# Optimization experiments

Hardware: AMD Instinct MI355X
Metric: run time of the kernel (lower is better)

Reference implementation:

```python
import jax, jax.numpy as jnp
import numpy as np
from jax import lax

RANK = 2
INPUT_SIZE = 8
HIDDEN_SIZE = 1024
NUM_MIXTURES = 4
ALPHA = 0.1
BASE_SCALE = 500.0
D = 2 * RANK + INPUT_SIZE  # 12
BATCH, SEQ_LEN = 64, 512


def setup_inputs() -> dict:
    key = jax.random.key(0)
    k1, k2, k3, k4, k5 = jax.random.split(key, 5)
    return {
        "x": jax.random.normal(k1, (BATCH, SEQ_LEN, INPUT_SIZE), jnp.float32),
        "eps": jax.random.normal(k2, (NUM_MIXTURES, HIDDEN_SIZE, D), jnp.float32),
        "means": jax.random.normal(k3, (NUM_MIXTURES, D), jnp.float32),
        "scale_tril_raw": jax.random.normal(k4, (NUM_MIXTURES, D, D), jnp.float32) / np.sqrt(HIDDEN_SIZE),
        "mixture_weights": jax.random.uniform(k5, (NUM_MIXTURES,), jnp.float32),
    }


def reference(x, eps, means, scale_tril_raw, mixture_weights):
    # _clamp_tril: lower-triangular with strictly positive diagonal
    diag = jnp.abs(jnp.diagonal(scale_tril_raw, axis1=-2, axis2=-1) - 1e-12) + 1e-12  # [K,D]
    L = jnp.tril(scale_tril_raw, -1) + diag[..., None] * jnp.eye(D, dtype=scale_tril_raw.dtype)
    # _normalize_weights
    w = jnp.clip(mixture_weights, 1e-6, None)
    w = w / jnp.sum(w)
    # rsample: mean + eps @ L^T, per mixture -> [K, H, D]
    samp = means[:, None, :] + jnp.einsum('khd,ked->khe', eps, L)
    mixed = jnp.einsum('k,khd->hd', w, samp)  # weighted sum over mixtures [H, D]
    m = mixed[:, :RANK]            # [H, r]
    n = mixed[:, RANK:2 * RANK]    # [H, r]
    I = mixed[:, 2 * RANK:]        # [H, input_size]
    J = (m @ n.T) * (BASE_SCALE / HIDDEN_SIZE)  # [H, H]
    span = jnp.concatenate([m, I], axis=1)      # [H, r + input_size]

    def step(h, x_t):
        dh = -h + jnp.tanh(h) @ J.T + x_t @ I.T
        h_new = h + ALPHA * dh
        return h_new, h_new

    h0 = jnp.zeros((x.shape[0], HIDDEN_SIZE), x.dtype)
    _, hs = lax.scan(step, h0, jnp.swapaxes(x, 0, 1))  # hs: [T, B, H]
    hiddens = jnp.swapaxes(hs, 0, 1)                   # [B, T, H]
    pinv = jnp.linalg.pinv(span)                       # [r+input_size, H]
    return jnp.einsum('dh,bth->btd', pinv, hiddens)    # [B, T, r+input_size]
```

## Files before the change

### kernel.cpp

```cpp
#include <hip/hip_runtime.h>

#define HS   1024
#define SEQ  512
#define NBAT 64
#define INSZ 8
#define NM   4
#define DD   12

#define DPP_ADD(v, ctrl, rmask, bmask) \
  v += __int_as_float(__builtin_amdgcn_update_dpp(0, __float_as_int(v), ctrl, rmask, bmask, true))

__device__ __forceinline__ void wave64_sum2(float &a, float &b){
  DPP_ADD(a, 0x111, 0xf, 0xf); DPP_ADD(b, 0x111, 0xf, 0xf);
  DPP_ADD(a, 0x112, 0xf, 0xf); DPP_ADD(b, 0x112, 0xf, 0xf);
  DPP_ADD(a, 0x114, 0xf, 0xe); DPP_ADD(b, 0x114, 0xf, 0xe);
  DPP_ADD(a, 0x118, 0xf, 0xc); DPP_ADD(b, 0x118, 0xf, 0xc);
  DPP_ADD(a, 0x142, 0xa, 0xf); DPP_ADD(b, 0x142, 0xa, 0xf);
  DPP_ADD(a, 0x143, 0xc, 0xf); DPP_ADD(b, 0x143, 0xc, 0xf);
}

__device__ __forceinline__ float fast_tanh(float x){
  float e = __expf(x + x);
  float r = __builtin_amdgcn_rcpf(e + 1.0f);
  return __builtin_fmaf(-2.0f, r, 1.0f);
}

__global__ __launch_bounds__(256,1)
void rnn_scan(const float* __restrict__ x,
              const float* __restrict__ eps,
              const float* __restrict__ means,
              const float* __restrict__ tril,
              const float* __restrict__ mw,
              float* __restrict__ out)
{
  const int b    = blockIdx.x;
  const int tid  = threadIdx.x;
  const int wave = tid >> 6;
  const int lane = tid & 63;

  __shared__ float  xs[SEQ*INSZ];
  __shared__ float2 red[2][4];
  __shared__ __align__(16) float outb[SEQ*10];

  float w[NM];
  {
    float s = 0.f;
    #pragma unroll
    for (int k=0;k<NM;k++){ w[k] = fmaxf(mw[k], 1e-6f); s += w[k]; }
    float inv = 1.0f/s;
    #pragma unroll
    for (int k=0;k<NM;k++) w[k] *= inv;
  }

  float m0[4],m1[4],n0[4],n1[4],h[4];
  float2 Im2[4][4];
  #pragma unroll
  for (int j=0;j<4;j++){
    const int i = tid + j*256;
    float ep[NM][DD];
    #pragma unroll
    for (int k=0;k<NM;k++)
      #pragma unroll
      for (int d=0;d<DD;d++)
        ep[k][d] = eps[(k*HS + i)*DD + d];
    float mix[DD];
    #pragma unroll
    for (int e=0;e<DD;e++){
      float a = 0.f;
      #pragma unroll
      for (int k=0;k<NM;k++){
        float se = means[k*DD+e];
        for (int d=0; d<e; d++)
          se += ep[k][d]*tril[(k*DD+e)*DD + d];
        float dg = fabsf(tril[(k*DD+e)*DD + e] - 1e-12f) + 1e-12f;
        se += ep[k][e]*dg;
        a += w[k]*se;
      }
      mix[e] = a;
    }
    m0[j]=mix[0]; m1[j]=mix[1]; n0[j]=mix[2]; n1[j]=mix[3];
    #pragma unroll
    for (int e=0;e<4;e++) Im2[j][e]=make_float2(mix[4+2*e], mix[5+2*e]);
    h[j]=0.f;
  }

  for (int idx=tid; idx<SEQ*INSZ; idx+=256) xs[idx] = x[b*SEQ*INSZ + idx];
  __syncthreads();

  const float alpha = 0.1f;
  const float oma   = 0.9f;
  const float scl   = 500.0f/1024.0f;
  const float as    = alpha*scl;
  float o = 0.f;
  const float2* xs2 = (const float2*)xs;

  #pragma unroll 2
  for (int t=0;t<SEQ;t++){
    float u0=0.f, u1=0.f;
    #pragma unroll
    for (int j=0;j<4;j++){
      float th = fast_tanh(h[j]);
      u0 = __builtin_fmaf(th, n0[j], u0);
      u1 = __builtin_fmaf(th, n1[j], u1);
    }
    wave64_sum2(u0, u1);
    if (lane==63) red[t&1][wave] = make_float2(u0,u1);

    float inj[4];
    #pragma unroll
    for (int j=0;j<4;j++){
      float2 acc = make_float2(0.f,0.f);
      #pragma unroll
      for (int e=0;e<4;e++){
        float2 xe = xs2[t*4+e];
        acc.x = __builtin_fmaf(xe.x, Im2[j][e].x, acc.x);
        acc.y = __builtin_fmaf(xe.y, Im2[j][e].y, acc.y);
      }
      inj[j] = acc.x + acc.y;
    }

    __syncthreads();
    float2 r0=red[t&1][0], r1=red[t&1][1], r2=red[t&1][2], r3=red[t&1][3];
    float U0 = (r0.x+r1.x)+(r2.x+r3.x);
    float U1 = (r0.y+r1.y)+(r2.y+r3.y);

    #pragma unroll
    for (int j=0;j<4;j++){
      float mu = __builtin_fmaf(m1[j], U1, m0[j]*U0);
      h[j] = __builtin_fmaf(oma, h[j],
             __builtin_fmaf(as, mu, alpha*inj[j]));
    }

    if (tid < 10){
      float add = (tid==0) ? scl*U0 : (tid==1) ? scl*U1 : xs[t*8 + tid-2];
      o = __builtin_fmaf(oma, o, alpha*add);
      outb[t*10+tid] = o;
    }
  }

  __syncthreads();
  const float4* ob4 = (const float4*)outb;
  float4* o4 = (float4*)out + b*(SEQ*10/4);
  for (int idx=tid; idx<SEQ*10/4; idx+=256) o4[idx] = ob4[idx];
}

extern "C" void kernel_launch(void* const* d_in, const int* in_sizes, int n_in,
                              void* d_out, int out_size, void* d_ws, size_t ws_size,
                              hipStream_t stream) {
  const float* x     = (const float*)d_in[0];
  const float* eps   = (const float*)d_in[1];
  const float* means = (const float*)d_in[2];
  const float* tril  = (const float*)d_in[3];
  const float* mw    = (const float*)d_in[4];
  float* out = (float*)d_out;

  rnn_scan<<<NBAT, 256, 0, stream>>>(x, eps, means, tril, mw, out);
}
```

Baseline: 290.8 us.

## Replace per-step barrier with tagged LDS flag polling and fold tanh algebra

The per-timestep __syncthreads is replaced by tagged 64-bit LDS slots: each wave's lane 63 writes its partial sums with the step index in the high bits, and every wave spins until all four slots carry the current tag, then combines them with DPP. The hidden state is kept as 2h so tanh becomes 1-2/(e^g+1), and the constant term is pre-summed into N0/N1 so each element needs one exp and one rcp. The input-injection terms are prescaled and the next step's x values are prefetched. The eight input-only output channels move out of the loop into a separate serial pass at the end. In exchange the code relies on volatile LDS polling with no barrier, which adds correctness risk and spin overhead.

```diff
diff --git a/kernel.cpp b/kernel.cpp
--- a/kernel.cpp
+++ b/kernel.cpp
@@ -17,12 +17,6 @@
   DPP_ADD(a, 0x118, 0xf, 0xc); DPP_ADD(b, 0x118, 0xf, 0xc);
   DPP_ADD(a, 0x142, 0xa, 0xf); DPP_ADD(b, 0x142, 0xa, 0xf);
   DPP_ADD(a, 0x143, 0xc, 0xf); DPP_ADD(b, 0x143, 0xc, 0xf);
-}
-
-__device__ __forceinline__ float fast_tanh(float x){
-  float e = __expf(x + x);
-  float r = __builtin_amdgcn_rcpf(e + 1.0f);
-  return __builtin_fmaf(-2.0f, r, 1.0f);
 }
 
 __global__ __launch_bounds__(256,1)
@@ -38,9 +32,10 @@
   const int wave = tid >> 6;
   const int lane = tid & 63;
 
-  __shared__ float  xs[SEQ*INSZ];
-  __shared__ float2 red[2][4];
+  __shared__ __align__(16) float xs[SEQ*INSZ + 8];
   __shared__ __align__(16) float outb[SEQ*10];
+  __shared__ unsigned long long red[2][4][2];
+  __shared__ float2 nsum[4];
 
   float w[NM];
   {
@@ -52,7 +47,13 @@
     for (int k=0;k<NM;k++) w[k] *= inv;
   }
 
-  float m0[4],m1[4],n0[4],n1[4],h[4];
+  const float alpha = 0.1f;
+  const float oma   = 0.9f;
+  const float scl   = 500.0f/1024.0f;
+  const float as2   = 2.0f*alpha*scl;
+  const float a2    = 2.0f*alpha;
+
+  float A0[4],A1[4],n0[4],n1[4],g[4];
   float2 Im2[4][4];
   #pragma unroll
   for (int j=0;j<4;j++){
@@ -78,67 +79,108 @@
       }
       mix[e] = a;
     }
-    m0[j]=mix[0]; m1[j]=mix[1]; n0[j]=mix[2]; n1[j]=mix[3];
-    #pragma unroll
-    for (int e=0;e<4;e++) Im2[j][e]=make_float2(mix[4+2*e], mix[5+2*e]);
-    h[j]=0.f;
-  }
-
+    A0[j]=as2*mix[0]; A1[j]=as2*mix[1]; n0[j]=mix[2]; n1[j]=mix[3];
+    #pragma unroll
+    for (int e=0;e<4;e++) Im2[j][e]=make_float2(a2*mix[4+2*e], a2*mix[5+2*e]);
+    g[j]=0.f;
+  }
+
+  {
+    float p0 = n0[0]+n0[1]+n0[2]+n0[3];
+    float p1 = n1[0]+n1[1]+n1[2]+n1[3];
+    wave64_sum2(p0,p1);
+    if (lane==63) nsum[wave] = make_float2(p0,p1);
+  }
+  if (tid < 16) ((unsigned long long*)red)[tid] = ~0ull;
   for (int idx=tid; idx<SEQ*INSZ; idx+=256) xs[idx] = x[b*SEQ*INSZ + idx];
   __syncthreads();
 
-  const float alpha = 0.1f;
-  const float oma   = 0.9f;
-  const float scl   = 500.0f/1024.0f;
-  const float as    = alpha*scl;
-  float o = 0.f;
+  const float N0 = (nsum[0].x+nsum[1].x)+(nsum[2].x+nsum[3].x);
+  const float N1 = (nsum[0].y+nsum[1].y)+(nsum[2].y+nsum[3].y);
+
   const float2* xs2 = (const float2*)xs;
+  volatile unsigned long long (*vred)[4][2] =
+      (volatile unsigned long long (*)[4][2])red;
+  const int w4 = lane & 3;
+
+  float o0=0.f, o1=0.f;
+  float2 xt[4];
+  #pragma unroll
+  for (int e=0;e<4;e++) xt[e] = xs2[e];
 
   #pragma unroll 2
   for (int t=0;t<SEQ;t++){
-    float u0=0.f, u1=0.f;
+    const int p = t&1;
+    float S0=0.f, S1=0.f;
     #pragma unroll
     for (int j=0;j<4;j++){
-      float th = fast_tanh(h[j]);
-      u0 = __builtin_fmaf(th, n0[j], u0);
-      u1 = __builtin_fmaf(th, n1[j], u1);
-    }
-    wave64_sum2(u0, u1);
-    if (lane==63) red[t&1][wave] = make_float2(u0,u1);
+      float e = __expf(g[j]);
+      float r = __builtin_amdgcn_rcpf(e + 1.0f);
+      S0 = __builtin_fmaf(r, n0[j], S0);
+      S1 = __builtin_fmaf(r, n1[j], S1);
+    }
+    wave64_sum2(S0,S1);
+    {
+      unsigned long long tagw = ((unsigned long long)(unsigned)t) << 32;
+      unsigned long long q0 = tagw | __float_as_uint(S0);
+      unsigned long long q1 = tagw | __float_as_uint(S1);
+      if (lane==63){ vred[p][wave][0]=q0; vred[p][wave][1]=q1; }
+    }
 
     float inj[4];
     #pragma unroll
     for (int j=0;j<4;j++){
-      float2 acc = make_float2(0.f,0.f);
-      #pragma unroll
-      for (int e=0;e<4;e++){
-        float2 xe = xs2[t*4+e];
-        acc.x = __builtin_fmaf(xe.x, Im2[j][e].x, acc.x);
-        acc.y = __builtin_fmaf(xe.y, Im2[j][e].y, acc.y);
-      }
-      inj[j] = acc.x + acc.y;
-    }
-
-    __syncthreads();
-    float2 r0=red[t&1][0], r1=red[t&1][1], r2=red[t&1][2], r3=red[t&1][3];
-    float U0 = (r0.x+r1.x)+(r2.x+r3.x);
-    float U1 = (r0.y+r1.y)+(r2.y+r3.y);
+      float ax = __builtin_fmaf(xt[0].x, Im2[j][0].x, xt[1].x*Im2[j][1].x);
+      float ay = __builtin_fmaf(xt[0].y, Im2[j][0].y, xt[1].y*Im2[j][1].y);
+      ax = __builtin_fmaf(xt[2].x, Im2[j][2].x, ax);
+      ay = __builtin_fmaf(xt[2].y, Im2[j][2].y, ay);
+      ax = __builtin_fmaf(xt[3].x, Im2[j][3].x, ax);
+      ay = __builtin_fmaf(xt[3].y, Im2[j][3].y, ay);
+      inj[j] = ax + ay;
+    }
+    float2 xtn[4];
+    #pragma unroll
+    for (int e=0;e<4;e++) xtn[e] = xs2[(t+1)*4 + e];
+
+    unsigned long long a, c;
+    for (int spin=0; spin<(1<<20); ++spin){
+      a = vred[p][w4][0];
+      c = vred[p][w4][1];
+      if (__all(((unsigned)(a>>32))==(unsigned)t &&
+                ((unsigned)(c>>32))==(unsigned)t)) break;
+    }
+    float s0 = __uint_as_float((unsigned)a);
+    float s1 = __uint_as_float((unsigned)c);
+    DPP_ADD(s0, 0xB1, 0xf, 0xf); DPP_ADD(s1, 0xB1, 0xf, 0xf);
+    DPP_ADD(s0, 0x4E, 0xf, 0xf); DPP_ADD(s1, 0x4E, 0xf, 0xf);
+    float U0 = __builtin_fmaf(-2.0f, s0, N0);
+    float U1 = __builtin_fmaf(-2.0f, s1, N1);
 
     #pragma unroll
     for (int j=0;j<4;j++){
-      float mu = __builtin_fmaf(m1[j], U1, m0[j]*U0);
-      h[j] = __builtin_fmaf(oma, h[j],
-             __builtin_fmaf(as, mu, alpha*inj[j]));
-    }
-
-    if (tid < 10){
-      float add = (tid==0) ? scl*U0 : (tid==1) ? scl*U1 : xs[t*8 + tid-2];
-      o = __builtin_fmaf(oma, o, alpha*add);
-      outb[t*10+tid] = o;
-    }
-  }
-
+      float acc = __builtin_fmaf(A1[j], U1, inj[j]);
+      acc = __builtin_fmaf(A0[j], U0, acc);
+      g[j] = __builtin_fmaf(oma, g[j], acc);
+    }
+
+    if (tid==0){
+      o0 = __builtin_fmaf(oma, o0, (alpha*scl)*U0);
+      o1 = __builtin_fmaf(oma, o1, (alpha*scl)*U1);
+      *(float2*)&outb[t*10] = make_float2(o0,o1);
+    }
+    #pragma unroll
+    for (int e=0;e<4;e++) xt[e] = xtn[e];
+  }
+
+  if (tid < 8){
+    float o = 0.f;
+    for (int t=0;t<SEQ;t++){
+      o = __builtin_fmaf(oma, o, alpha*xs[t*8+tid]);
+      outb[t*10+2+tid] = o;
+    }
+  }
   __syncthreads();
+
   const float4* ob4 = (const float4*)outb;
   float4* o4 = (float4*)out + b*(SEQ*10/4);
   for (int idx=tid; idx<SEQ*10/4; idx+=256) o4[idx] = ob4[idx];
```

New measurement: 297.3 us. +2.2%, slower.
